# Optimization experiments

Hardware: AMD Instinct MI355X
Metric: run time of the kernel (lower is better)

The kernel has to match this reference:

```python
import jax, jax.numpy as jnp
import numpy as np


def conv1d_same(x, w, b, dilation=1):
    # x: [B, T, Cin], w: [K, Cin, Cout] (WIO), 'same' padding, stride 1
    y = jax.lax.conv_general_dilated(
        x, w, window_strides=(1,), padding='SAME',
        rhs_dilation=(dilation,), dimension_numbers=('NWC', 'WIO', 'NWC'))
    return y + b


def setup_inputs() -> dict:
    key = jax.random.key(0)
    ks = jax.random.split(key, 6)
    B, T, N_IN, N_OUT, ATTN_DIM, KSZ = 16, 2048, 96, 128, 64, 3
    return {
        'x': jax.random.normal(ks[0], (B, T, N_IN), jnp.float32),
        'qkv_w': jax.random.normal(ks[1], (N_IN, 3 * ATTN_DIM), jnp.float32) * 0.05,
        'qkv_b': jnp.zeros((3 * ATTN_DIM,), jnp.float32),
        'scale': jnp.ones((), jnp.float32),
        'conv_w1': jax.random.normal(ks[2], (KSZ, ATTN_DIM, N_OUT), jnp.float32) * 0.05,
        'conv_b1': jnp.zeros((N_OUT,), jnp.float32),
        'conv_w2': jax.random.normal(ks[3], (KSZ, N_OUT, N_OUT), jnp.float32) * 0.05,
        'conv_b2': jnp.zeros((N_OUT,), jnp.float32),
        'down_w': jax.random.normal(ks[4], (N_IN, N_OUT), jnp.float32) * 0.1,
    }


def reference(x, qkv_w, qkv_b, scale, conv_w1, conv_b1, conv_w2, conv_b2, down_w):
    # Dense4Attention: single Dense(3*attn_dim), split into q,k,v
    qkv = x @ qkv_w + qkv_b                       # [B,T,3*D]
    q, k, v = jnp.split(qkv, 3, axis=-1)          # each [B,T,D]
    # AttentionBlock: scores = q k^T * learned scale; non-causal (default)
    scores = jnp.einsum('btd,bsd->bts', q, k) * scale   # [B,T,T]
    weights = jax.nn.softmax(scores, axis=2)            # softmax_axis=2
    out_attn = jnp.einsum('bts,bsd->btd', weights, v)   # [B,T,D]
    h = jax.nn.relu(conv1d_same(out_attn, conv_w1, conv_b1, 1))
    out = jax.nn.relu(conv1d_same(h, conv_w2, conv_b2, 1))   # [B,T,n_out]
    # enhanced residual: softmax over time of row-sums of attn weights
    weight_x = jax.nn.softmax(jnp.sum(weights, axis=2), axis=1)  # [B,T]
    en_res_x = (weight_x[..., None] * x) @ down_w   # n_in != n_out -> downsample
    res = x @ down_w                                 # skip path downsample
    return jax.nn.relu(out + res + en_res_x)
```

## Files before the change

### kernel.cpp

```cpp
#include <hip/hip_runtime.h>
#include <cstdint>

#define B_   16
#define T_   2048
#define CIN  96
#define DH   64
#define NOUT 128

typedef float floatx4 __attribute__((ext_vector_type(4)));
typedef short shortx8 __attribute__((ext_vector_type(8)));
typedef unsigned int uintx2 __attribute__((ext_vector_type(2)));

__device__ __forceinline__ unsigned short f2bf(float f) {
  unsigned int u = __float_as_uint(f);
  u += 0x7FFFu + ((u >> 16) & 1u);
  return (unsigned short)(u >> 16);
}
__device__ __forceinline__ uint32_t pack_bf2(float lo, float hi) {
  return (uint32_t)f2bf(lo) | ((uint32_t)f2bf(hi) << 16);
}
__device__ __forceinline__ floatx4 f4zero() { floatx4 v; v[0]=0.f;v[1]=0.f;v[2]=0.f;v[3]=0.f; return v; }
__device__ __forceinline__ shortx8 s8zero() { shortx8 v;
#pragma unroll
  for (int i=0;i<8;++i) v[i]=0; return v; }

__device__ __forceinline__ void plane_swap(uint32_t& a, uint32_t& b) {
#if __has_builtin(__builtin_amdgcn_permlane32_swap) && __has_builtin(__builtin_amdgcn_permlane16_swap)
  uintx2 r1 = __builtin_amdgcn_permlane32_swap(a, b, false, false);
  uintx2 r2 = __builtin_amdgcn_permlane16_swap(r1[0], r1[1], false, false);
  a = r2[0]; b = r2[1];
#else
  asm volatile("v_permlane32_swap_b32 %0, %1\n\t"
               "v_permlane16_swap_b32 %0, %1"
               : "+v"(a), "+v"(b));
#endif
}

__global__ __launch_bounds__(256) void k_wprep(
    const float* __restrict__ qkv_w, const float* __restrict__ cw1,
    const float* __restrict__ cw2, const float* __restrict__ dw,
    unsigned short* __restrict__ qwt, unsigned short* __restrict__ w1t,
    unsigned short* __restrict__ w2t, unsigned short* __restrict__ dwt)
{
  int o = blockIdx.x * 256 + threadIdx.x;
  if (o < 18432) {
    int co = o / 96, ci = o % 96;
    qwt[o] = f2bf(qkv_w[ci * 192 + co]);
  } else if (o < 43008) {
    int p = o - 18432;
    int tap = p / 8192, rem = p % 8192, co = rem >> 6, ci = rem & 63;
    w1t[p] = f2bf(cw1[(tap * 64 + ci) * 128 + co]);
  } else if (o < 92160) {
    int p = o - 43008;
    int tap = p / 16384, rem = p % 16384, co = rem >> 7, ci = rem & 127;
    w2t[p] = f2bf(cw2[(tap * 128 + ci) * 128 + co]);
  } else if (o < 104448) {
    int p = o - 92160;
    int co = p / 96, ci = p % 96;
    dwt[p] = f2bf(dw[ci * 128 + co]);
  }
}

__global__ __launch_bounds__(256) void k_qkv(
    const float* __restrict__ x, const unsigned short* __restrict__ qwt,
    const float* __restrict__ qkv_b, const float* __restrict__ scale_p,
    unsigned short* __restrict__ qb, unsigned short* __restrict__ kb,
    unsigned short* __restrict__ vT)
{
  __shared__ __align__(16) unsigned short Xs[64][104];
  const int bx = blockIdx.x;
  const int b = bx >> 5, t0 = (bx & 31) * 64;
  const int tid = threadIdx.x, wave = tid >> 6, lane = tid & 63;
  const int l15 = lane & 15, quad = lane >> 4;
  const float scl2 = scale_p[0] * 1.4426950408889634f;

  for (int idx = tid; idx < 64 * 24; idx += 256) {
    int r = idx / 24, c = (idx % 24) * 4;
    float4 xv = *(const float4*)(x + ((size_t)(b * T_ + t0 + r)) * CIN + c);
    ushort4 o; o.x = f2bf(xv.x); o.y = f2bf(xv.y); o.z = f2bf(xv.z); o.w = f2bf(xv.w);
    *(ushort4*)(&Xs[r][c]) = o;
  }
  __syncthreads();

  floatx4 acc[4][3];
#pragma unroll
  for (int mt = 0; mt < 4; ++mt)
#pragma unroll
    for (int nt = 0; nt < 3; ++nt) acc[mt][nt] = f4zero();

#pragma unroll
  for (int ks = 0; ks < 3; ++ks) {
    shortx8 wf[3];
#pragma unroll
    for (int nt = 0; nt < 3; ++nt) {
      int j = wave * 48 + nt * 16 + l15;
      wf[nt] = *(const shortx8*)(qwt + (size_t)j * 96 + ks * 32 + quad * 8);
    }
#pragma unroll
    for (int mt = 0; mt < 4; ++mt) {
      shortx8 af = *(const shortx8*)(&Xs[mt * 16 + l15][ks * 32 + quad * 8]);
#pragma unroll
      for (int nt = 0; nt < 3; ++nt)
        acc[mt][nt] = __builtin_amdgcn_mfma_f32_16x16x32_bf16(af, wf[nt], acc[mt][nt], 0, 0, 0);
    }
  }

#pragma unroll
  for (int nt = 0; nt < 3; ++nt) {
    int j0 = wave * 48 + nt * 16;
    int j = j0 + l15;
    float bias = qkv_b[j];
#pragma unroll
    for (int mt = 0; mt < 4; ++mt) {
#pragma unroll
      for (int r = 0; r < 4; ++r) {
        int t = t0 + mt * 16 + quad * 4 + r;
        float v = acc[mt][nt][r] + bias;
        if (j0 < 64)        qb[((size_t)b * T_ + t) * DH + j] = f2bf(v * scl2);
        else if (j0 < 128)  kb[((size_t)b * T_ + t) * DH + (j - 64)] = f2bf(v);
        else                vT[((size_t)b * DH + (j - 128)) * T_ + t] = f2bf(v);
      }
    }
  }
}

__global__ __launch_bounds__(256) void k_attn(
    const unsigned short* __restrict__ qb, const unsigned short* __restrict__ kb,
    const unsigned short* __restrict__ vT,
    float* __restrict__ opart, float* __restrict__ lws)
{
  __shared__ __align__(16) unsigned short Kt[64][72];
  __shared__ __align__(16) unsigned short Vt[80][72];
  const int bx = blockIdx.x;
  const int half = bx & 1, qt = (bx >> 1) & 31, b = bx >> 6;
  const int tid = threadIdx.x, wave = tid >> 6, lane = tid & 63;
  const int l15 = lane & 15, quad = lane >> 4;

  const unsigned short* qrow = qb + ((size_t)b * T_ + qt * 64 + wave * 16 + l15) * DH;
  shortx8 qf0 = *(const shortx8*)(qrow + quad * 8);
  shortx8 qf1 = *(const shortx8*)(qrow + 32 + quad * 8);

  floatx4 O[5];
#pragma unroll
  for (int i = 0; i < 5; ++i) O[i] = f4zero();

  const unsigned short* kbase = kb + (size_t)b * T_ * DH + (size_t)half * 1024 * DH;
  const unsigned short* vbase = vT + (size_t)b * DH * T_ + half * 1024;

  for (int idx = tid; idx < 16 * 72; idx += 256) {
    int r = idx / 72, c = idx % 72;
    Vt[64 + r][c] = (r == 0) ? (unsigned short)0x3F80 : (unsigned short)0;
  }

  const int kr0 = tid >> 3, kc = (tid & 7) * 8;
  shortx8 pk[2], pv[2];
#pragma unroll
  for (int i = 0; i < 2; ++i) {
    pk[i] = *(const shortx8*)(kbase + (size_t)(kr0 + i * 32) * DH + kc);
    pv[i] = *(const shortx8*)(vbase + (size_t)(kr0 + i * 32) * T_ + kc);
  }

  for (int t = 0; t < 16; ++t) {
#pragma unroll
    for (int i = 0; i < 2; ++i) {
      *(shortx8*)(&Kt[kr0 + i * 32][kc]) = pk[i];
      *(shortx8*)(&Vt[kr0 + i * 32][kc]) = pv[i];
    }
    __syncthreads();

    if (t < 15) {
      int s0 = (t + 1) * 64;
#pragma unroll
      for (int i = 0; i < 2; ++i) {
        pk[i] = *(const shortx8*)(kbase + (size_t)(s0 + kr0 + i * 32) * DH + kc);
        pv[i] = *(const shortx8*)(vbase + (size_t)(kr0 + i * 32) * T_ + s0 + kc);
      }
    }

    floatx4 S[4];
#pragma unroll
    for (int nt = 0; nt < 4; ++nt) {
      shortx8 bk0 = *(const shortx8*)(&Kt[nt * 16 + l15][quad * 8]);
      shortx8 bk1 = *(const shortx8*)(&Kt[nt * 16 + l15][32 + quad * 8]);
      S[nt] = f4zero();
      S[nt] = __builtin_amdgcn_mfma_f32_16x16x32_bf16(bk0, qf0, S[nt], 0, 0, 0);
      S[nt] = __builtin_amdgcn_mfma_f32_16x16x32_bf16(bk1, qf1, S[nt], 0, 0, 0);
    }

    uint32_t pkv[8];
#pragma unroll
    for (int nt = 0; nt < 4; ++nt) {
#pragma unroll
      for (int j = 0; j < 2; ++j)
        pkv[nt * 2 + j] = pack_bf2(exp2f(S[nt][2 * j]), exp2f(S[nt][2 * j + 1]));
    }

#pragma unroll
    for (int kk = 0; kk < 2; ++kk) {
      uint32_t a0 = pkv[4 * kk + 0], b0 = pkv[4 * kk + 2];
      plane_swap(a0, b0);
      uint32_t a1 = pkv[4 * kk + 1], b1 = pkv[4 * kk + 3];
      plane_swap(a1, b1);
      union { shortx8 s; uint32_t u[4]; } fu;
      fu.u[0] = a0; fu.u[1] = a1; fu.u[2] = b0; fu.u[3] = b1;
#pragma unroll
      for (int dt = 0; dt < 5; ++dt) {
        shortx8 bv = *(const shortx8*)(&Vt[dt * 16 + l15][kk * 32 + quad * 8]);
        O[dt] = __builtin_amdgcn_mfma_f32_16x16x32_bf16(fu.s, bv, O[dt], 0, 0, 0);
      }
    }
    __syncthreads();
  }

  float* obase = opart + (((size_t)(half * B_ + b) * T_) + qt * 64 + wave * 16) * DH;
#pragma unroll
  for (int r = 0; r < 4; ++r) {
    int row = quad * 4 + r;
#pragma unroll
    for (int dt = 0; dt < 4; ++dt)
      obase[(size_t)row * DH + dt * 16 + l15] = O[dt][r];
    if (l15 == 0)
      lws[half * (B_ * T_) + b * T_ + qt * 64 + wave * 16 + row] = O[4][r];
  }
}

__global__ __launch_bounds__(256) void k_conv1(
    const float* __restrict__ opart, const float* __restrict__ lws,
    const unsigned short* __restrict__ w1t, const float* __restrict__ b1,
    unsigned short* __restrict__ hb)
{
  __shared__ __align__(16) unsigned short At[66][72];
  const int bx = blockIdx.x;
  const int b = bx >> 5, t0 = (bx & 31) * 64;
  const int tid = threadIdx.x, wave = tid >> 6, lane = tid & 63;
  const int l15 = lane & 15, quad = lane >> 4;
  const size_t HS = (size_t)B_ * T_ * DH;

  for (int idx = tid; idx < 66 * 8; idx += 256) {
    int r = idx >> 3, c = (idx & 7) * 8;
    int t = t0 + r - 1;
    shortx8 v = s8zero();
    if (t >= 0 && t < T_) {
      size_t bt = (size_t)b * T_ + t;
      const float* p0 = opart + bt * DH + c;
      const float* p1 = opart + HS + bt * DH + c;
      float inv = 1.f / (lws[bt] + lws[B_ * T_ + bt]);
      float4 a0 = *(const float4*)(p0), a1 = *(const float4*)(p0 + 4);
      float4 c0 = *(const float4*)(p1), c1 = *(const float4*)(p1 + 4);
      v[0] = (short)f2bf((a0.x + c0.x) * inv);
      v[1] = (short)f2bf((a0.y + c0.y) * inv);
      v[2] = (short)f2bf((a0.z + c0.z) * inv);
      v[3] = (short)f2bf((a0.w + c0.w) * inv);
      v[4] = (short)f2bf((a1.x + c1.x) * inv);
      v[5] = (short)f2bf((a1.y + c1.y) * inv);
      v[6] = (short)f2bf((a1.z + c1.z) * inv);
      v[7] = (short)f2bf((a1.w + c1.w) * inv);
    }
    *(shortx8*)(&At[r][c]) = v;
  }
  __syncthreads();

  floatx4 acc[4][2];
#pragma unroll
  for (int mt = 0; mt < 4; ++mt) { acc[mt][0] = f4zero(); acc[mt][1] = f4zero(); }

#pragma unroll
  for (int tap = 0; tap < 3; ++tap) {
#pragma unroll
    for (int ks = 0; ks < 2; ++ks) {
      shortx8 wf[2];
#pragma unroll
      for (int ct = 0; ct < 2; ++ct) {
        int co = wave * 32 + ct * 16 + l15;
        wf[ct] = *(const shortx8*)(w1t + ((size_t)tap * 128 + co) * 64 + ks * 32 + quad * 8);
      }
#pragma unroll
      for (int mt = 0; mt < 4; ++mt) {
        shortx8 af = *(const shortx8*)(&At[mt * 16 + l15 + tap][ks * 32 + quad * 8]);
        acc[mt][0] = __builtin_amdgcn_mfma_f32_16x16x32_bf16(af, wf[0], acc[mt][0], 0, 0, 0);
        acc[mt][1] = __builtin_amdgcn_mfma_f32_16x16x32_bf16(af, wf[1], acc[mt][1], 0, 0, 0);
      }
    }
  }

#pragma unroll
  for (int ct = 0; ct < 2; ++ct) {
    int co = wave * 32 + ct * 16 + l15;
    float bias = b1[co];
#pragma unroll
    for (int mt = 0; mt < 4; ++mt)
#pragma unroll
      for (int r = 0; r < 4; ++r) {
        int t = t0 + mt * 16 + quad * 4 + r;
        hb[((size_t)b * T_ + t) * NOUT + co] = f2bf(fmaxf(acc[mt][ct][r] + bias, 0.f));
      }
  }
}

__global__ __launch_bounds__(256) void k_conv2(
    const unsigned short* __restrict__ hb, const float* __restrict__ x,
    const unsigned short* __restrict__ w2t, const unsigned short* __restrict__ dwt,
    const float* __restrict__ b2, float* __restrict__ out)
{
  __shared__ __align__(16) unsigned short Ht[66][136];
  __shared__ __align__(16) unsigned short Xt[64][104];
  const int bx = blockIdx.x;
  const int b = bx >> 5, t0 = (bx & 31) * 64;
  const int tid = threadIdx.x, wave = tid >> 6, lane = tid & 63;
  const int l15 = lane & 15, quad = lane >> 4;

  for (int idx = tid; idx < 66 * 16; idx += 256) {
    int r = idx >> 4, c = (idx & 15) * 8;
    int t = t0 + r - 1;
    shortx8 v = s8zero();
    if (t >= 0 && t < T_) v = *(const shortx8*)(hb + ((size_t)b * T_ + t) * NOUT + c);
    *(shortx8*)(&Ht[r][c]) = v;
  }
  for (int idx = tid; idx < 64 * 24; idx += 256) {
    int r = idx / 24, c = (idx % 24) * 4;
    float4 xv = *(const float4*)(x + ((size_t)(b * T_ + t0 + r)) * CIN + c);
    ushort4 o; o.x = f2bf(xv.x); o.y = f2bf(xv.y); o.z = f2bf(xv.z); o.w = f2bf(xv.w);
    *(ushort4*)(&Xt[r][c]) = o;
  }
  __syncthreads();

  floatx4 a2[4][2], ar[4][2];
#pragma unroll
  for (int mt = 0; mt < 4; ++mt) { a2[mt][0]=f4zero(); a2[mt][1]=f4zero(); ar[mt][0]=f4zero(); ar[mt][1]=f4zero(); }

#pragma unroll
  for (int tap = 0; tap < 3; ++tap) {
#pragma unroll
    for (int ks = 0; ks < 4; ++ks) {
      shortx8 wf[2];
#pragma unroll
      for (int ct = 0; ct < 2; ++ct) {
        int co = wave * 32 + ct * 16 + l15;
        wf[ct] = *(const shortx8*)(w2t + ((size_t)tap * 128 + co) * 128 + ks * 32 + quad * 8);
      }
#pragma unroll
      for (int mt = 0; mt < 4; ++mt) {
        shortx8 af = *(const shortx8*)(&Ht[mt * 16 + l15 + tap][ks * 32 + quad * 8]);
        a2[mt][0] = __builtin_amdgcn_mfma_f32_16x16x32_bf16(af, wf[0], a2[mt][0], 0, 0, 0);
        a2[mt][1] = __builtin_amdgcn_mfma_f32_16x16x32_bf16(af, wf[1], a2[mt][1], 0, 0, 0);
      }
    }
  }
#pragma unroll
  for (int ks = 0; ks < 3; ++ks) {
    shortx8 wf[2];
#pragma unroll
    for (int ct = 0; ct < 2; ++ct) {
      int co = wave * 32 + ct * 16 + l15;
      wf[ct] = *(const shortx8*)(dwt + (size_t)co * 96 + ks * 32 + quad * 8);
    }
#pragma unroll
    for (int mt = 0; mt < 4; ++mt) {
      shortx8 af = *(const shortx8*)(&Xt[mt * 16 + l15][ks * 32 + quad * 8]);
      ar[mt][0] = __builtin_amdgcn_mfma_f32_16x16x32_bf16(af, wf[0], ar[mt][0], 0, 0, 0);
      ar[mt][1] = __builtin_amdgcn_mfma_f32_16x16x32_bf16(af, wf[1], ar[mt][1], 0, 0, 0);
    }
  }

  const float kres = 1.0f + 1.0f / 2048.0f;
#pragma unroll
  for (int ct = 0; ct < 2; ++ct) {
    int co = wave * 32 + ct * 16 + l15;
    float bias = b2[co];
#pragma unroll
    for (int mt = 0; mt < 4; ++mt)
#pragma unroll
      for (int r = 0; r < 4; ++r) {
        int t = t0 + mt * 16 + quad * 4 + r;
        float o2 = fmaxf(a2[mt][ct][r] + bias, 0.f);
        out[((size_t)b * T_ + t) * NOUT + co] = fmaxf(o2 + ar[mt][ct][r] * kres, 0.f);
      }
  }
}

extern "C" void kernel_launch(void* const* d_in, const int* in_sizes, int n_in,
                              void* d_out, int out_size, void* d_ws, size_t ws_size,
                              hipStream_t stream) {
  const float* x      = (const float*)d_in[0];
  const float* qkv_w  = (const float*)d_in[1];
  const float* qkv_b  = (const float*)d_in[2];
  const float* scale  = (const float*)d_in[3];
  const float* cw1    = (const float*)d_in[4];
  const float* cb1    = (const float*)d_in[5];
  const float* cw2    = (const float*)d_in[6];
  const float* cb2    = (const float*)d_in[7];
  const float* dw     = (const float*)d_in[8];

  char* ws = (char*)d_ws;
  unsigned short* qb  = (unsigned short*)(ws + 0);
  unsigned short* kb  = (unsigned short*)(ws + 4194304);
  unsigned short* vT  = (unsigned short*)(ws + 8388608);
  unsigned short* hb  = (unsigned short*)(ws + 16777216);
  unsigned short* qwt = (unsigned short*)(ws + 25165824);
  unsigned short* w1t = (unsigned short*)(ws + 25202688);
  unsigned short* w2t = (unsigned short*)(ws + 25251840);
  unsigned short* dwt = (unsigned short*)(ws + 25350144);
  float*          lws = (float*)(ws + 25374720);

  float* opart = (float*)d_out;

  k_wprep<<<408, 256, 0, stream>>>(qkv_w, cw1, cw2, dw, qwt, w1t, w2t, dwt);
  k_qkv  <<<512, 256, 0, stream>>>(x, qwt, qkv_b, scale, qb, kb, vT);
  k_attn <<<1024, 256, 0, stream>>>(qb, kb, vT, opart, lws);
  k_conv1<<<512, 256, 0, stream>>>(opart, lws, w1t, cb1, hb);
  k_conv2<<<512, 256, 0, stream>>>(hb, x, w2t, dwt, cb2, (float*)d_out);
}
```

Measured before the change: 148.9 us.

## Give each attention wave two query tiles and compute row sums in registers

The attention kernel now runs 2 waves per block, each handling 32 query rows (two 16-row groups). Each K/V fragment read from shared memory therefore feeds twice as many MFMAs. The extra ones-row in the V tile, which previously produced the softmax row sums through a fifth MFMA, is removed. Row sums are instead accumulated in fp32 from the exponentials and reduced with lane shuffles. This cuts LDS traffic and MFMA work per output, at the cost of fewer threads per block, more registers per thread, and more global-load work per thread when staging K/V.

```diff
diff --git a/kernel.cpp b/kernel.cpp
--- a/kernel.cpp
+++ b/kernel.cpp
@@ -124,103 +124,132 @@
   }
 }
 
-__global__ __launch_bounds__(256) void k_attn(
+__global__ __launch_bounds__(128) void k_attn(
     const unsigned short* __restrict__ qb, const unsigned short* __restrict__ kb,
     const unsigned short* __restrict__ vT,
     float* __restrict__ opart, float* __restrict__ lws)
 {
   __shared__ __align__(16) unsigned short Kt[64][72];
-  __shared__ __align__(16) unsigned short Vt[80][72];
+  __shared__ __align__(16) unsigned short Vt[64][72];
   const int bx = blockIdx.x;
   const int half = bx & 1, qt = (bx >> 1) & 31, b = bx >> 6;
   const int tid = threadIdx.x, wave = tid >> 6, lane = tid & 63;
   const int l15 = lane & 15, quad = lane >> 4;
 
-  const unsigned short* qrow = qb + ((size_t)b * T_ + qt * 64 + wave * 16 + l15) * DH;
-  shortx8 qf0 = *(const shortx8*)(qrow + quad * 8);
-  shortx8 qf1 = *(const shortx8*)(qrow + 32 + quad * 8);
-
-  floatx4 O[5];
-#pragma unroll
-  for (int i = 0; i < 5; ++i) O[i] = f4zero();
+  const unsigned short* qrow = qb + ((size_t)b * T_ + qt * 64 + wave * 32 + l15) * DH;
+  shortx8 qf[2][2];
+  qf[0][0] = *(const shortx8*)(qrow + quad * 8);
+  qf[0][1] = *(const shortx8*)(qrow + 32 + quad * 8);
+  qf[1][0] = *(const shortx8*)(qrow + (size_t)16 * DH + quad * 8);
+  qf[1][1] = *(const shortx8*)(qrow + (size_t)16 * DH + 32 + quad * 8);
+
+  floatx4 O[2][4];
+#pragma unroll
+  for (int qg = 0; qg < 2; ++qg)
+#pragma unroll
+    for (int dt = 0; dt < 4; ++dt) O[qg][dt] = f4zero();
+  float lsum[2] = {0.f, 0.f};
 
   const unsigned short* kbase = kb + (size_t)b * T_ * DH + (size_t)half * 1024 * DH;
   const unsigned short* vbase = vT + (size_t)b * DH * T_ + half * 1024;
 
-  for (int idx = tid; idx < 16 * 72; idx += 256) {
-    int r = idx / 72, c = idx % 72;
-    Vt[64 + r][c] = (r == 0) ? (unsigned short)0x3F80 : (unsigned short)0;
-  }
-
-  const int kr0 = tid >> 3, kc = (tid & 7) * 8;
-  shortx8 pk[2], pv[2];
-#pragma unroll
-  for (int i = 0; i < 2; ++i) {
-    pk[i] = *(const shortx8*)(kbase + (size_t)(kr0 + i * 32) * DH + kc);
-    pv[i] = *(const shortx8*)(vbase + (size_t)(kr0 + i * 32) * T_ + kc);
+  const int sr = tid & 63, sh = (tid >> 6) * 32;
+  shortx8 pk[4], pv[4];
+#pragma unroll
+  for (int i = 0; i < 4; ++i) {
+    pk[i] = *(const shortx8*)(kbase + (size_t)sr * DH + sh + i * 8);
+    pv[i] = *(const shortx8*)(vbase + (size_t)sr * T_ + sh + i * 8);
   }
 
   for (int t = 0; t < 16; ++t) {
 #pragma unroll
-    for (int i = 0; i < 2; ++i) {
-      *(shortx8*)(&Kt[kr0 + i * 32][kc]) = pk[i];
-      *(shortx8*)(&Vt[kr0 + i * 32][kc]) = pv[i];
+    for (int i = 0; i < 4; ++i) {
+      *(shortx8*)(&Kt[sr][sh + i * 8]) = pk[i];
+      *(shortx8*)(&Vt[sr][sh + i * 8]) = pv[i];
     }
     __syncthreads();
 
     if (t < 15) {
       int s0 = (t + 1) * 64;
 #pragma unroll
-      for (int i = 0; i < 2; ++i) {
-        pk[i] = *(const shortx8*)(kbase + (size_t)(s0 + kr0 + i * 32) * DH + kc);
-        pv[i] = *(const shortx8*)(vbase + (size_t)(kr0 + i * 32) * T_ + s0 + kc);
-      }
-    }
-
-    floatx4 S[4];
+      for (int i = 0; i < 4; ++i) {
+        pk[i] = *(const shortx8*)(kbase + (size_t)(s0 + sr) * DH + sh + i * 8);
+        pv[i] = *(const shortx8*)(vbase + (size_t)sr * T_ + s0 + sh + i * 8);
+      }
+    }
+
+    floatx4 S[2][4];
 #pragma unroll
     for (int nt = 0; nt < 4; ++nt) {
       shortx8 bk0 = *(const shortx8*)(&Kt[nt * 16 + l15][quad * 8]);
       shortx8 bk1 = *(const shortx8*)(&Kt[nt * 16 + l15][32 + quad * 8]);
-      S[nt] = f4zero();
-      S[nt] = __builtin_amdgcn_mfma_f32_16x16x32_bf16(bk0, qf0, S[nt], 0, 0, 0);
-      S[nt] = __builtin_amdgcn_mfma_f32_16x16x32_bf16(bk1, qf1, S[nt], 0, 0, 0);
-    }
-
-    uint32_t pkv[8];
-#pragma unroll
-    for (int nt = 0; nt < 4; ++nt) {
-#pragma unroll
-      for (int j = 0; j < 2; ++j)
-        pkv[nt * 2 + j] = pack_bf2(exp2f(S[nt][2 * j]), exp2f(S[nt][2 * j + 1]));
-    }
+#pragma unroll
+      for (int qg = 0; qg < 2; ++qg) {
+        floatx4 s = f4zero();
+        s = __builtin_amdgcn_mfma_f32_16x16x32_bf16(bk0, qf[qg][0], s, 0, 0, 0);
+        s = __builtin_amdgcn_mfma_f32_16x16x32_bf16(bk1, qf[qg][1], s, 0, 0, 0);
+        S[qg][nt] = s;
+      }
+    }
+
+    uint32_t pkv[2][8];
+#pragma unroll
+    for (int qg = 0; qg < 2; ++qg)
+#pragma unroll
+      for (int nt = 0; nt < 4; ++nt)
+#pragma unroll
+        for (int j = 0; j < 2; ++j) {
+          float lo = exp2f(S[qg][nt][2 * j]);
+          float hi = exp2f(S[qg][nt][2 * j + 1]);
+          lsum[qg] += lo + hi;
+          pkv[qg][nt * 2 + j] = pack_bf2(lo, hi);
+        }
 
 #pragma unroll
     for (int kk = 0; kk < 2; ++kk) {
-      uint32_t a0 = pkv[4 * kk + 0], b0 = pkv[4 * kk + 2];
-      plane_swap(a0, b0);
-      uint32_t a1 = pkv[4 * kk + 1], b1 = pkv[4 * kk + 3];
-      plane_swap(a1, b1);
-      union { shortx8 s; uint32_t u[4]; } fu;
-      fu.u[0] = a0; fu.u[1] = a1; fu.u[2] = b0; fu.u[3] = b1;
-#pragma unroll
-      for (int dt = 0; dt < 5; ++dt) {
+      shortx8 fu[2];
+#pragma unroll
+      for (int qg = 0; qg < 2; ++qg) {
+        uint32_t a0 = pkv[qg][4 * kk + 0], b0 = pkv[qg][4 * kk + 2];
+        plane_swap(a0, b0);
+        uint32_t a1 = pkv[qg][4 * kk + 1], b1 = pkv[qg][4 * kk + 3];
+        plane_swap(a1, b1);
+        union { shortx8 s; uint32_t u[4]; } f;
+        f.u[0] = a0; f.u[1] = a1; f.u[2] = b0; f.u[3] = b1;
+        fu[qg] = f.s;
+      }
+#pragma unroll
+      for (int dt = 0; dt < 4; ++dt) {
         shortx8 bv = *(const shortx8*)(&Vt[dt * 16 + l15][kk * 32 + quad * 8]);
-        O[dt] = __builtin_amdgcn_mfma_f32_16x16x32_bf16(fu.s, bv, O[dt], 0, 0, 0);
+        O[0][dt] = __builtin_amdgcn_mfma_f32_16x16x32_bf16(fu[0], bv, O[0][dt], 0, 0, 0);
+        O[1][dt] = __builtin_amdgcn_mfma_f32_16x16x32_bf16(fu[1], bv, O[1][dt], 0, 0, 0);
       }
     }
     __syncthreads();
   }
 
-  float* obase = opart + (((size_t)(half * B_ + b) * T_) + qt * 64 + wave * 16) * DH;
-#pragma unroll
-  for (int r = 0; r < 4; ++r) {
-    int row = quad * 4 + r;
-#pragma unroll
-    for (int dt = 0; dt < 4; ++dt)
-      obase[(size_t)row * DH + dt * 16 + l15] = O[dt][r];
-    if (l15 == 0)
-      lws[half * (B_ * T_) + b * T_ + qt * 64 + wave * 16 + row] = O[4][r];
+  float* obase = opart + (((size_t)(half * B_ + b) * T_) + qt * 64 + wave * 32) * DH;
+#pragma unroll
+  for (int qg = 0; qg < 2; ++qg)
+#pragma unroll
+    for (int r = 0; r < 4; ++r) {
+      int row = qg * 16 + quad * 4 + r;
+#pragma unroll
+      for (int dt = 0; dt < 4; ++dt)
+        obase[(size_t)row * DH + dt * 16 + l15] = O[qg][dt][r];
+    }
+
+#pragma unroll
+  for (int qg = 0; qg < 2; ++qg) {
+    float v = lsum[qg];
+    v += __shfl_xor(v, 16);
+    v += __shfl_xor(v, 32);
+    lsum[qg] = v;
+  }
+  if (lane < 16) {
+    size_t base = (size_t)half * (B_ * T_) + (size_t)b * T_ + qt * 64 + wave * 32;
+    lws[base + lane] = lsum[0];
+    lws[base + 16 + lane] = lsum[1];
   }
 }
 
@@ -406,7 +435,7 @@
 
   k_wprep<<<408, 256, 0, stream>>>(qkv_w, cw1, cw2, dw, qwt, w1t, w2t, dwt);
   k_qkv  <<<512, 256, 0, stream>>>(x, qwt, qkv_b, scale, qb, kb, vT);
-  k_attn <<<1024, 256, 0, stream>>>(qb, kb, vT, opart, lws);
+  k_attn <<<1024, 128, 0, stream>>>(qb, kb, vT, opart, lws);
   k_conv1<<<512, 256, 0, stream>>>(opart, lws, w1t, cb1, hb);
   k_conv2<<<512, 256, 0, stream>>>(hb, x, w2t, dwt, cb2, (float*)d_out);
 }
```

Result: slower. 156.6 us (+5.2%).
